# Performance work log

Hardware: AMD Instinct MI355X
Metric: run time of the kernel (lower is better)

Reference implementation:

```python
import jax, jax.numpy as jnp
import numpy as np

L = 10          # number of integration steps
MU = 0.02       # residual intensity weight
SIGMA = 2.0     # Gaussian RKHS sigma (voxels)
KS = 13         # kernel size ~ 2*ceil(3*sigma)+1
SLOPE = 0.01    # LeakyReLU default negative slope
HID = 50


def _gauss1d():
    r = jnp.arange(KS, dtype=jnp.float32) - (KS - 1) / 2.0
    k = jnp.exp(-0.5 * (r / SIGMA) ** 2)
    return k / k.sum()


def gaussian_smooth(x):
    # x: [B,C,D,H,W]; separable Gaussian RKHS smoothing, zero ('constant') border
    B, C, D, H, W = x.shape
    k = _gauss1d().astype(x.dtype)
    y = x.reshape(B * C, 1, D, H, W)
    p = (KS - 1) // 2
    dn = ('NCDHW', 'OIDHW', 'NCDHW')
    y = jax.lax.conv_general_dilated(y, k.reshape(1, 1, KS, 1, 1), (1, 1, 1), [(p, p), (0, 0), (0, 0)], dimension_numbers=dn)
    y = jax.lax.conv_general_dilated(y, k.reshape(1, 1, 1, KS, 1), (1, 1, 1), [(0, 0), (p, p), (0, 0)], dimension_numbers=dn)
    y = jax.lax.conv_general_dilated(y, k.reshape(1, 1, 1, 1, KS), (1, 1, 1), [(0, 0), (0, 0), (p, p)], dimension_numbers=dn)
    return y.reshape(B, C, D, H, W)


def spatial_gradient_3d(img):
    # img [B,1,D,H,W] -> [B,1,3,D,H,W]; central differences, replicate pad; channels (d/dx=W, d/dy=H, d/dz=D)
    def cd(axis):
        pad = [(0, 0)] * 5
        pad[axis] = (1, 1)
        p = jnp.pad(img, pad, mode='edge')
        sp = [slice(None)] * 5
        sm = [slice(None)] * 5
        sp[axis] = slice(2, None)
        sm[axis] = slice(0, -2)
        return 0.5 * (p[tuple(sp)] - p[tuple(sm)])
    return jnp.stack([cd(4), cd(3), cd(2)], axis=2)


def grid_sample_3d(img, grid):
    # trilinear grid_sample, align_corners=True, border padding
    # img [B,C,D,H,W]; grid [B,Do,Ho,Wo,3] with normalized (x,y,z) -> (W,H,D)
    B, C, D, H, W = img.shape
    Do, Ho, Wo = grid.shape[1:4]
    x = jnp.clip((grid[..., 0] + 1.0) * 0.5 * (W - 1), 0.0, W - 1.0)
    y = jnp.clip((grid[..., 1] + 1.0) * 0.5 * (H - 1), 0.0, H - 1.0)
    z = jnp.clip((grid[..., 2] + 1.0) * 0.5 * (D - 1), 0.0, D - 1.0)
    x0 = jnp.floor(x); y0 = jnp.floor(y); z0 = jnp.floor(z)
    x1 = jnp.minimum(x0 + 1.0, W - 1.0)
    y1 = jnp.minimum(y0 + 1.0, H - 1.0)
    z1 = jnp.minimum(z0 + 1.0, D - 1.0)
    wx = x - x0; wy = y - y0; wz = z - z0
    imgf = img.reshape(B, C, D * H * W)

    def gather(zi, yi, xi):
        idx = ((zi * H + yi) * W + xi).astype(jnp.int32).reshape(B, 1, -1)
        return jnp.take_along_axis(imgf, idx, axis=2)

    out = 0.0
    for zi, wzc in ((z0, 1.0 - wz), (z1, wz)):
        for yi, wyc in ((y0, 1.0 - wy), (y1, wy)):
            for xi, wxc in ((x0, 1.0 - wx), (x1, wx)):
                w8 = (wzc * wyc * wxc).reshape(B, 1, -1)
                out = out + gather(zi, yi, xi) * w8
    return out.reshape(B, C, Do, Ho, Wo)


def conv3d(x, w):
    return jax.lax.conv_general_dilated(x, w, (1, 1, 1), [(1, 1)] * 3, dimension_numbers=('NCDHW', 'OIDHW', 'NCDHW'))


def res_block(w1, w2, w3, z, I, J):
    # dropout is identity at inference
    x = jnp.concatenate([z, I, J], axis=1)
    x = jax.nn.leaky_relu(conv3d(x, w1), SLOPE)
    x = jax.nn.leaky_relu(conv3d(x, w2), SLOPE)
    return conv3d(x, w3)


def identity_grid(D, H, W):
    xs = jnp.linspace(-1.0, 1.0, W)
    ys = jnp.linspace(-1.0, 1.0, H)
    zs = jnp.linspace(-1.0, 1.0, D)
    zg, yg, xg = jnp.meshgrid(zs, ys, xs, indexing='ij')
    return jnp.stack([xg, yg, zg], axis=-1)[None]  # [1,D,H,W,3]


def metamorph_forward(source, target, source_seg, z0, W1, W2, W3):
    B = source.shape[0]
    D, H, W = source.shape[2:]
    id_grid = identity_grid(D, H, W)
    residual = jnp.broadcast_to(z0, (B,) + z0.shape[1:])
    res_def = jnp.zeros_like(source)
    phi = jnp.broadcast_to(id_grid, (B, D, H, W, 3))
    image = source
    fields, grads, residuals = [], [], [residual]
    for i in range(L):
        g = spatial_gradient_3d(image)                 # [B,1,3,D,H,W]
        grads.append(g)
        v = gaussian_smooth(-residual * g[:, 0])       # [B,3,D,H,W]
        field = jnp.transpose(v, (0, 4, 3, 2, 1))      # [B,W,H,D,3] (cubic volume)
        deformation = id_grid - field / L
        f = res_block(W1[i], W2[i], W3[i], residual, image, target) / L
        residual = residual + f
        residuals.append(residual)
        if i > 0:
            res_def = grid_sample_3d(res_def, deformation)
        res_def = res_def + residual
        phi = jnp.transpose(grid_sample_3d(jnp.transpose(phi, (0, 4, 3, 2, 1)), deformation), (0, 4, 3, 2, 1))
        mask = grid_sample_3d(source_seg, phi)
        image = grid_sample_3d(source, phi) + res_def * (MU ** 2 / L) * mask
        fields.append(field)
    return image, jnp.stack(fields), jnp.stack(grads), jnp.stack(residuals), res_def


def setup_inputs() -> dict:
    key = jax.random.key(0)
    ks = jax.random.split(key, 7)
    B, D = 1, 64
    return {
        "source": jax.random.normal(ks[0], (B, 1, D, D, D), jnp.float32),
        "target": jax.random.normal(ks[1], (B, 1, D, D, D), jnp.float32),
        "source_seg": jax.random.uniform(ks[2], (B, 1, D, D, D), jnp.float32),
        "z0": 0.1 * jax.random.normal(ks[3], (1, 1, D, D, D), jnp.float32),
        "W1": 0.05 * jax.random.normal(ks[4], (L, HID, 3, 3, 3, 3), jnp.float32),
        "W2": 0.05 * jax.random.normal(ks[5], (L, HID, HID, 3, 3, 3), jnp.float32),
        "W3": 0.05 * jax.random.normal(ks[6], (L, 1, HID, 3, 3, 3), jnp.float32),
    }


def reference(source, target, source_seg, z0, W1, W2, W3):
    return metamorph_forward(source, target, source_seg, z0, W1, W2, W3)
```

## Files before the change

### kernel.cpp

```cpp
#include <hip/hip_runtime.h>

#define NV 262144

using bf16x8 = __attribute__((ext_vector_type(8))) short;
using f32x4  = __attribute__((ext_vector_type(4))) float;

typedef const __attribute__((address_space(1))) unsigned int* gua_t;
typedef __attribute__((address_space(3))) unsigned int* lua_t;

static __device__ __forceinline__ void gld16(const void* g, void* l) {
  __builtin_amdgcn_global_load_lds((gua_t)g, (lua_t)l, 16, 0, 0);
}

static __device__ __forceinline__ unsigned short f2bf(float x) {
  unsigned int u = __float_as_uint(x);
  unsigned int r = (u + 0x7FFFu + ((u >> 16) & 1u)) >> 16;
  return (unsigned short)r;
}

static __device__ __forceinline__ void gauss_weights(float K[13]) {
  float s = 0.f;
#pragma unroll
  for (int j = 0; j < 13; ++j) {
    float r = (float)(j - 6);
    K[j] = expf(-0.125f * r * r);
    s += K[j];
  }
#pragma unroll
  for (int j = 0; j < 13; ++j) K[j] = K[j] / s;
}

static __device__ __forceinline__ void tl_make(float gx, float gy, float gz,
                                               int sx, int sy, int sz,
                                               int id[8], float wt[8]) {
  float x = fminf(fmaxf((gx + 1.0f) * 0.5f * 63.0f, 0.0f), 63.0f);
  float y = fminf(fmaxf((gy + 1.0f) * 0.5f * 63.0f, 0.0f), 63.0f);
  float z = fminf(fmaxf((gz + 1.0f) * 0.5f * 63.0f, 0.0f), 63.0f);
  float x0f = floorf(x), y0f = floorf(y), z0f = floorf(z);
  int x0 = (int)x0f, y0 = (int)y0f, z0 = (int)z0f;
  int x1 = min(x0 + 1, 63), y1 = min(y0 + 1, 63), z1 = min(z0 + 1, 63);
  float wx = x - x0f, wy = y - y0f, wz = z - z0f;
  float ux = 1.f - wx, uy = 1.f - wy, uz = 1.f - wz;
  int X0 = x0 * sx, X1 = x1 * sx, Y0 = y0 * sy, Y1 = y1 * sy, Z0 = z0 * sz, Z1 = z1 * sz;
  id[0] = Z0 + Y0 + X0; wt[0] = uz * uy * ux;
  id[1] = Z0 + Y0 + X1; wt[1] = uz * uy * wx;
  id[2] = Z0 + Y1 + X0; wt[2] = uz * wy * ux;
  id[3] = Z0 + Y1 + X1; wt[3] = uz * wy * wx;
  id[4] = Z1 + Y0 + X0; wt[4] = wz * uy * ux;
  id[5] = Z1 + Y0 + X1; wt[5] = wz * uy * wx;
  id[6] = Z1 + Y1 + X0; wt[6] = wz * wy * ux;
  id[7] = Z1 + Y1 + X1; wt[7] = wz * wy * wx;
}

static __device__ __forceinline__ float tl_apply(const float* __restrict__ img,
                                                 const int id[8], const float wt[8]) {
  float s = 0.f;
#pragma unroll
  for (int k = 0; k < 8; ++k) s = fmaf(wt[k], img[id[k]], s);
  return s;
}

__global__ void init_kernel(const float* __restrict__ src, const float* __restrict__ tgt,
                            const float* __restrict__ z0,
                            float* __restrict__ residual, float* __restrict__ image,
                            float* __restrict__ rd0, float* __restrict__ phi0,
                            float* __restrict__ outRes0, unsigned short* __restrict__ cinb,
                            float* __restrict__ zpf) {
  int idx = blockIdx.x * 256 + threadIdx.x;
  int d = idx >> 12, h = (idx >> 6) & 63, w = idx & 63;
  float z = z0[idx];
  float sv = src[idx];
  residual[idx] = z;
  outRes0[idx] = z;
  image[idx] = sv;
  rd0[idx] = 0.f;
  const float step = 2.0f / 63.0f;
  phi0[idx] = -1.f + w * step;
  phi0[NV + idx] = -1.f + h * step;
  phi0[2 * NV + idx] = -1.f + d * step;
  unsigned int u0 = (unsigned int)f2bf(z) | ((unsigned int)f2bf(sv) << 16);
  unsigned int u1 = (unsigned int)f2bf(tgt[idx]);
  *(uint2*)(cinb + (size_t)idx * 4) = make_uint2(u0, u1);
  if (idx < 32) zpf[idx] = 0.f;
}

__global__ void gsd_kernel(const float* __restrict__ img, const float* __restrict__ residual,
                           float* __restrict__ gout, float* __restrict__ t1) {
  int idx = blockIdx.x * 256 + threadIdx.x;
  int d = idx >> 12, h = (idx >> 6) & 63, w = idx & 63;
  float K[13]; gauss_weights(K);
  int wp = min(w + 1, 63), wm = max(w - 1, 0);
  int hp = min(h + 1, 63), hm = max(h - 1, 0);
  float a0 = 0.f, a1 = 0.f, a2 = 0.f;
#pragma unroll
  for (int j = 0; j < 13; ++j) {
    int dd = d + j - 6;
    if ((unsigned)dd < 64u) {
      int b = (dd << 12) + (h << 6);
      int dp = min(dd + 1, 63), dm = max(dd - 1, 0);
      float gx = 0.5f * (img[b + wp] - img[b + wm]);
      float gy = 0.5f * (img[(dd << 12) + (hp << 6) + w] - img[(dd << 12) + (hm << 6) + w]);
      float gz = 0.5f * (img[(dp << 12) + (h << 6) + w] - img[(dm << 12) + (h << 6) + w]);
      float r = residual[b + w];
      if (j == 6) {
        gout[idx] = gx; gout[NV + idx] = gy; gout[2 * NV + idx] = gz;
      }
      a0 = fmaf(K[j], -r * gx, a0);
      a1 = fmaf(K[j], -r * gy, a1);
      a2 = fmaf(K[j], -r * gz, a2);
    }
  }
  t1[idx] = a0; t1[NV + idx] = a1; t1[2 * NV + idx] = a2;
}

__global__ __launch_bounds__(256) void smooth_hw(const float* __restrict__ t1,
                                                 float* __restrict__ vbuf,
                                                 float* __restrict__ fout) {
  __shared__ float shin[16][64];
  __shared__ float shh[4][64];
  int w = threadIdx.x & 63;
  int ty = threadIdx.x >> 6;
  int h0 = blockIdx.x * 4;
  int d  = blockIdx.y;
  float K[13]; gauss_weights(K);
  for (int c = 0; c < 3; ++c) {
    __syncthreads();
    const float* tc = t1 + (size_t)c * NV + (d << 12);
    for (int r = ty; r < 16; r += 4) {
      int hh = h0 - 6 + r;
      shin[r][w] = ((unsigned)hh < 64u) ? tc[(hh << 6) + w] : 0.f;
    }
    __syncthreads();
    float acc = 0.f;
#pragma unroll
    for (int j = 0; j < 13; ++j) {
      int hh = h0 + ty + j - 6;
      if ((unsigned)hh < 64u) acc = fmaf(K[j], shin[ty + j][w], acc);
    }
    shh[ty][w] = acc;
    __syncthreads();
    float o = 0.f;
#pragma unroll
    for (int j = 0; j < 13; ++j) {
      int wj = w + j - 6;
      if ((unsigned)wj < 64u) o = fmaf(K[j], shh[ty][wj], o);
    }
    int h = h0 + ty;
    vbuf[(size_t)c * NV + (d << 12) + (h << 6) + w] = o;
    fout[((size_t)(w << 12) + (h << 6) + d) * 3 + c] = o;
  }
}

#define MFMA_PREP_G(XB, ZP)                                                        \
  const unsigned short* gp[6];                                                     \
  _Pragma("unroll")                                                                \
  for (int k = 0; k < 6; ++k) {                                                    \
    int S = wv * 384 + k * 64 + lane;                                              \
    int wws = S % 18; int t = S / 18; int q = t & 1; int dhh = t >> 1;             \
    int hh = dhh % 6; int dd = dhh / 6;                                            \
    int gz = d0 + dd - 1, gy = h0 + hh - 1, gx = w0 + wws - 1;                     \
    bool ok = (S < 1296) && ((unsigned)gz < 64u) && ((unsigned)gy < 64u) && ((unsigned)gx < 64u); \
    gp[k] = ok ? ((XB) + ((((gz << 12) + (gy << 6) + gx) << 6) + q * 8)) : (ZP);   \
  }

#define MFMA_ISSUE(G, DSTBUF)                                                      \
  _Pragma("unroll")                                                                \
  for (int k = 0; k < 6; ++k)                                                      \
    gld16(gp[k] + (G) * 16, (DSTBUF) + wv * 6144 + k * 1024);

#define TAP_ADDR                                                                   \
  int tap = 2 * c + (kb >> 1);                                                     \
  int tapc = min(tap, 26);                                                         \
  int kd = (tapc * 57) >> 9;                                                       \
  int rem = tapc - kd * 9;                                                         \
  int kh = (rem * 43) >> 7;                                                        \
  int kw = rem - kh * 3;                                                           \
  int rb = ((kd * 6 + kh) * 2 + (kb & 1)) * 288 + kw * 16;

#define MFMA_BLOCKID                                                               \
  int f = blockIdx.x + 4 * (blockIdx.y + 16 * blockIdx.z);                         \
  int nid = (f & 7) * 128 + (f >> 3);                                              \
  const int w0 = (nid & 3) * 16, h0 = ((nid >> 2) & 15) * 4, d0 = (nid >> 6) * 4;

#define MFMA_EPILOGUE(ACC, XOUT)                                                   \
  _Pragma("unroll")                                                                \
  for (int nf = 0; nf < 4; ++nf) {                                                 \
    int idx = ((d0 + wv) << 12) + ((h0 + nf) << 6) + (w0 + ww);                    \
    unsigned int base = (unsigned int)idx * 64u + kb * 4u;                         \
    _Pragma("unroll")                                                              \
    for (int mf = 0; mf < 4; ++mf) {                                               \
      float v0 = ACC[mf][nf][0], v1 = ACC[mf][nf][1];                              \
      float v2 = ACC[mf][nf][2], v3 = ACC[mf][nf][3];                              \
      v0 = (v0 >= 0.f) ? v0 : 0.01f * v0;                                          \
      v1 = (v1 >= 0.f) ? v1 : 0.01f * v1;                                          \
      v2 = (v2 >= 0.f) ? v2 : 0.01f * v2;                                          \
      v3 = (v3 >= 0.f) ? v3 : 0.01f * v3;                                          \
      unsigned int u0 = (unsigned int)f2bf(v0) | ((unsigned int)f2bf(v1) << 16);   \
      unsigned int u1 = (unsigned int)f2bf(v2) | ((unsigned int)f2bf(v3) << 16);   \
      *(uint2*)((XOUT) + base + mf * 16u) = make_uint2(u0, u1);                    \
    }                                                                              \
  }

__global__ __launch_bounds__(256) void conv1_mfma(const unsigned short* __restrict__ cinb,
                                                  const unsigned short* __restrict__ w1m,
                                                  unsigned short* __restrict__ x1b) {
  __shared__ char sh[1296 * 8];
  const int tid = threadIdx.x;
  const int lane = tid & 63;
  const int wv = tid >> 6;
  const int ww = lane & 15;
  const int kb = lane >> 4;
  MFMA_BLOCKID

  int gofs[6]; int lofs[6]; bool gok[6]; bool sval[6];
#pragma unroll
  for (int k = 0; k < 6; ++k) {
    int s = tid + k * 256;
    sval[k] = (s < 1296);
    int wws = s % 18; int rest = s / 18;
    int hh = rest % 6; int dd = rest / 6;
    int gz = d0 + dd - 1, gy = h0 + hh - 1, gx = w0 + wws - 1;
    bool ok = sval[k] && ((unsigned)gz < 64u) && ((unsigned)gy < 64u) && ((unsigned)gx < 64u);
    gok[k] = ok;
    gofs[k] = ok ? (((gz << 12) + (gy << 6) + gx) * 4) : 0;
    lofs[k] = s * 8;
  }
  {
    uint2 stg[6];
#pragma unroll
    for (int k = 0; k < 6; ++k)
      stg[k] = gok[k] ? *(const uint2*)(cinb + gofs[k]) : make_uint2(0u, 0u);
#pragma unroll
    for (int k = 0; k < 6; ++k)
      if (sval[k]) *(uint2*)(sh + lofs[k]) = stg[k];
  }
  __syncthreads();

  f32x4 acc[4][4];
#pragma unroll
  for (int mf = 0; mf < 4; ++mf)
#pragma unroll
    for (int nf = 0; nf < 4; ++nf) acc[mf][nf] = (f32x4)0.f;

#pragma unroll
  for (int g = 0; g < 4; ++g) {
    bf16x8 a0 = *(const bf16x8*)(w1m + (((g * 4 + 0) * 64 + lane) << 3));
    bf16x8 a1 = *(const bf16x8*)(w1m + (((g * 4 + 1) * 64 + lane) << 3));
    bf16x8 a2 = *(const bf16x8*)(w1m + (((g * 4 + 2) * 64 + lane) << 3));
    bf16x8 a3 = *(const bf16x8*)(w1m + (((g * 4 + 3) * 64 + lane) << 3));
    int tap0 = 8 * g + 2 * kb;
    int t0 = min(tap0, 26), t1 = min(tap0 + 1, 26);
    int kd0 = (t0 * 57) >> 9; int r0 = t0 - kd0 * 9; int kh0 = (r0 * 43) >> 7; int kw0 = r0 - kh0 * 3;
    int kd1 = (t1 * 57) >> 9; int r1 = t1 - kd1 * 9; int kh1 = (r1 * 43) >> 7; int kw1 = r1 - kh1 * 3;
#pragma unroll
    for (int nf = 0; nf < 4; ++nf) {
      union { uint2 u[2]; bf16x8 v; } bb;
      bb.u[0] = *(const uint2*)(sh + (((wv + kd0) * 6 + (nf + kh0)) * 18 + (ww + kw0)) * 8);
      bb.u[1] = *(const uint2*)(sh + (((wv + kd1) * 6 + (nf + kh1)) * 18 + (ww + kw1)) * 8);
      acc[0][nf] = __builtin_amdgcn_mfma_f32_16x16x32_bf16(a0, bb.v, acc[0][nf], 0, 0, 0);
      acc[1][nf] = __builtin_amdgcn_mfma_f32_16x16x32_bf16(a1, bb.v, acc[1][nf], 0, 0, 0);
      acc[2][nf] = __builtin_amdgcn_mfma_f32_16x16x32_bf16(a2, bb.v, acc[2][nf], 0, 0, 0);
      acc[3][nf] = __builtin_amdgcn_mfma_f32_16x16x32_bf16(a3, bb.v, acc[3][nf], 0, 0, 0);
    }
  }

  MFMA_EPILOGUE(acc, x1b)
}

__global__ __launch_bounds__(256) void conv2_mfma(const unsigned short* __restrict__ x1b,
                                                  const unsigned short* __restrict__ wtm,
                                                  unsigned short* __restrict__ x2b,
                                                  const unsigned short* __restrict__ zp) {
  __shared__ char sh[2][24576];
  const int tid = threadIdx.x;
  const int lane = tid & 63;
  const int wv = tid >> 6;
  const int ww = lane & 15;
  const int kb = lane >> 4;
  MFMA_BLOCKID

  MFMA_PREP_G(x1b, zp)

  f32x4 acc[4][4];
#pragma unroll
  for (int mf = 0; mf < 4; ++mf)
#pragma unroll
    for (int nf = 0; nf < 4; ++nf) acc[mf][nf] = (f32x4)0.f;

  const int nb0 = wv * 3456 + ww * 16;

  MFMA_ISSUE(0, sh[0])
  __syncthreads();

  for (int g = 0; g < 4; ++g) {
    if (g < 3) { MFMA_ISSUE(g + 1, sh[(g + 1) & 1]) }
    const char* buf = sh[g & 1];
#pragma unroll
    for (int c = 0; c < 14; ++c) {
      bf16x8 a0 = *(const bf16x8*)(wtm + ((((g * 14 + c) * 4 + 0) * 64 + lane) << 3));
      bf16x8 a1 = *(const bf16x8*)(wtm + ((((g * 14 + c) * 4 + 1) * 64 + lane) << 3));
      bf16x8 a2 = *(const bf16x8*)(wtm + ((((g * 14 + c) * 4 + 2) * 64 + lane) << 3));
      bf16x8 a3 = *(const bf16x8*)(wtm + ((((g * 14 + c) * 4 + 3) * 64 + lane) << 3));
      TAP_ADDR
      const char* bp = buf + nb0 + rb;
      bf16x8 b0 = *(const bf16x8*)(bp);
      bf16x8 b1 = *(const bf16x8*)(bp + 576);
      bf16x8 b2 = *(const bf16x8*)(bp + 2 * 576);
      bf16x8 b3 = *(const bf16x8*)(bp + 3 * 576);
#define MFMA_ROW(MF, AF)                                                              \
      acc[MF][0] = __builtin_amdgcn_mfma_f32_16x16x32_bf16(AF, b0, acc[MF][0], 0, 0, 0); \
      acc[MF][1] = __builtin_amdgcn_mfma_f32_16x16x32_bf16(AF, b1, acc[MF][1], 0, 0, 0); \
      acc[MF][2] = __builtin_amdgcn_mfma_f32_16x16x32_bf16(AF, b2, acc[MF][2], 0, 0, 0); \
      acc[MF][3] = __builtin_amdgcn_mfma_f32_16x16x32_bf16(AF, b3, acc[MF][3], 0, 0, 0);
      MFMA_ROW(0, a0)
      MFMA_ROW(1, a1)
      MFMA_ROW(2, a2)
      MFMA_ROW(3, a3)
#undef MFMA_ROW
    }
    __syncthreads();
  }

  MFMA_EPILOGUE(acc, x2b)
}

__global__ __launch_bounds__(256) void conv3_mfma(const unsigned short* __restrict__ x2b,
                                                  const unsigned short* __restrict__ w3m,
                                                  float* __restrict__ residual,
                                                  float* __restrict__ resOut,
                                                  const unsigned short* __restrict__ zp) {
  __shared__ char sh[2][24576];
  const int tid = threadIdx.x;
  const int lane = tid & 63;
  const int wv = tid >> 6;
  const int ww = lane & 15;
  const int kb = lane >> 4;
  MFMA_BLOCKID

  MFMA_PREP_G(x2b, zp)

  f32x4 acc[4];
#pragma unroll
  for (int nf = 0; nf < 4; ++nf) acc[nf] = (f32x4)0.f;

  const int nb0 = wv * 3456 + ww * 16;

  MFMA_ISSUE(0, sh[0])
  __syncthreads();

  for (int g = 0; g < 4; ++g) {
    if (g < 3) { MFMA_ISSUE(g + 1, sh[(g + 1) & 1]) }
    const char* buf = sh[g & 1];
#pragma unroll
    for (int c = 0; c < 14; ++c) {
      bf16x8 a0 = *(const bf16x8*)(w3m + (((g * 14 + c) * 64 + lane) << 3));
      TAP_ADDR
      const char* bp = buf + nb0 + rb;
      bf16x8 b0 = *(const bf16x8*)(bp);
      bf16x8 b1 = *(const bf16x8*)(bp + 576);
      bf16x8 b2 = *(const bf16x8*)(bp + 2 * 576);
      bf16x8 b3 = *(const bf16x8*)(bp + 3 * 576);
      acc[0] = __builtin_amdgcn_mfma_f32_16x16x32_bf16(a0, b0, acc[0], 0, 0, 0);
      acc[1] = __builtin_amdgcn_mfma_f32_16x16x32_bf16(a0, b1, acc[1], 0, 0, 0);
      acc[2] = __builtin_amdgcn_mfma_f32_16x16x32_bf16(a0, b2, acc[2], 0, 0, 0);
      acc[3] = __builtin_amdgcn_mfma_f32_16x16x32_bf16(a0, b3, acc[3], 0, 0, 0);
    }
    __syncthreads();
  }

  if (lane < 16) {
#pragma unroll
    for (int nf = 0; nf < 4; ++nf) {
      int idx = ((d0 + wv) << 12) + ((h0 + nf) << 6) + (w0 + ww);
      float nr = residual[idx] + acc[nf][0] * 0.1f;
      residual[idx] = nr;
      resOut[idx] = nr;
    }
  }
}

__global__ void rp_fused_kernel(const float* __restrict__ rdOld, const float* __restrict__ v,
                                const float* __restrict__ residual,
                                const float* __restrict__ phiOld, float* __restrict__ phiNew,
                                const float* __restrict__ src, const float* __restrict__ seg,
                                const float* __restrict__ tgt,
                                float* __restrict__ rdNew, float* __restrict__ image,
                                unsigned short* __restrict__ cinb, int doSample) {
  int idx = blockIdx.x * 256 + threadIdx.x;
  int d = idx >> 12, h = (idx >> 6) & 63, w = idx & 63;
  const float step = 2.0f / 63.0f;
  float rres = residual[idx];

  float val = 0.f;
  if (doSample) {
    int tidx = (w << 12) + (h << 6) + d;
    float gx = (-1.f + w * step) - v[tidx] / 10.0f;
    float gy = (-1.f + h * step) - v[NV + tidx] / 10.0f;
    float gz = (-1.f + d * step) - v[2 * NV + tidx] / 10.0f;
    int id[8]; float wt[8];
    tl_make(gx, gy, gz, 1, 64, 4096, id, wt);
    val = tl_apply(rdOld, id, wt);
  }
  float nr = val + rres;
  rdNew[idx] = nr;

  float gx = (-1.f + d * step) - v[idx] / 10.0f;
  float gy = (-1.f + h * step) - v[NV + idx] / 10.0f;
  float gz = (-1.f + w * step) - v[2 * NV + idx] / 10.0f;
  int id[8]; float wt[8];
  tl_make(gx, gy, gz, 4096, 64, 1, id, wt);
  float px = tl_apply(phiOld, id, wt);
  float py = tl_apply(phiOld + NV, id, wt);
  float pz = tl_apply(phiOld + 2 * NV, id, wt);
  phiNew[idx] = px;
  phiNew[NV + idx] = py;
  phiNew[2 * NV + idx] = pz;

  int id2[8]; float wt2[8];
  tl_make(px, py, pz, 1, 64, 4096, id2, wt2);
  float sval = tl_apply(src, id2, wt2);
  float mval = tl_apply(seg, id2, wt2);
  float img = sval + nr * 4.0e-05f * mval;
  image[idx] = img;

  unsigned int u0 = (unsigned int)f2bf(rres) | ((unsigned int)f2bf(img) << 16);
  unsigned int u1 = (unsigned int)f2bf(tgt[idx]);
  *(uint2*)(cinb + (size_t)idx * 4) = make_uint2(u0, u1);
}

__global__ void w1m_kernel(const float* __restrict__ W1, unsigned short* __restrict__ w1m) {
  int gid = blockIdx.x * 256 + threadIdx.x;
  if (gid >= 10 * 4 * 4 * 64 * 8) return;
  int j = gid & 7;
  int l = (gid >> 3) & 63;
  int mf = (gid >> 9) & 3;
  int g = (gid >> 11) & 3;
  int i = gid >> 13;
  int m = mf * 16 + (l & 15);
  int kb = l >> 4;
  int k = 32 * g + 8 * kb + j;
  int tap = k >> 2;
  int ci = k & 3;
  float v = 0.f;
  if (m < 50 && tap < 27 && ci < 3)
    v = W1[(((size_t)i * 50 + m) * 3 + ci) * 27 + tap];
  w1m[gid] = f2bf(v);
}

__global__ void wt2m_kernel(const float* __restrict__ W2, unsigned short* __restrict__ wtm) {
  int gid = blockIdx.x * 256 + threadIdx.x;
  if (gid >= 10 * 4 * 14 * 4 * 64 * 8) return;
  int j = gid & 7;
  int l = (gid >> 3) & 63;
  int mf = (gid >> 9) & 3;
  int rest = gid >> 11;
  int c = rest % 14; rest /= 14;
  int g = rest & 3;  int i = rest >> 2;
  int m = mf * 16 + (l & 15);
  int kb = l >> 4;
  int klocal = c * 32 + kb * 8 + j;
  int tap = klocal >> 4;
  int cil = klocal & 15;
  int ci = g * 16 + cil;
  float v = 0.f;
  if (tap < 27 && ci < 50 && m < 50)
    v = W2[(((size_t)i * 50 + m) * 50 + ci) * 27 + tap];
  wtm[gid] = f2bf(v);
}

__global__ void w3m_kernel(const float* __restrict__ W3, unsigned short* __restrict__ w3m) {
  int gid = blockIdx.x * 256 + threadIdx.x;
  if (gid >= 10 * 4 * 14 * 64 * 8) return;
  int j = gid & 7;
  int l = (gid >> 3) & 63;
  int rest = gid >> 9;
  int c = rest % 14; rest /= 14;
  int g = rest & 3;  int i = rest >> 2;
  int m = l & 15;
  int kb = l >> 4;
  int klocal = c * 32 + kb * 8 + j;
  int tap = klocal >> 4;
  int cil = klocal & 15;
  int ci = g * 16 + cil;
  float v = 0.f;
  if (m == 0 && tap < 27 && ci < 50)
    v = W3[((size_t)i * 50 + ci) * 27 + tap];
  w3m[gid] = f2bf(v);
}

extern "C" void kernel_launch(void* const* d_in, const int* in_sizes, int n_in,
                              void* d_out, int out_size, void* d_ws, size_t ws_size,
                              hipStream_t stream) {
  const float* src = (const float*)d_in[0];
  const float* tgt = (const float*)d_in[1];
  const float* seg = (const float*)d_in[2];
  const float* z0  = (const float*)d_in[3];
  const float* W1  = (const float*)d_in[4];
  const float* W2  = (const float*)d_in[5];
  const float* W3  = (const float*)d_in[6];
  float* out = (float*)d_out;
  float* ws = (float*)d_ws;

  const size_t N = NV;
  float* residual = ws;
  float* image    = ws + N;
  float* rdb[2]   = { ws + 2 * N, ws + 3 * N };
  float* phib[2]  = { ws + 4 * N, ws + 7 * N };
  float* vbuf     = ws + 10 * N;
  float* t1       = ws + 13 * N;
  unsigned short* cinb = (unsigned short*)(ws + 16 * N);
  unsigned short* x1b = (unsigned short*)(ws + 19 * N);
  unsigned short* x2b = (unsigned short*)(ws + 51 * N);
  unsigned short* wt2m = (unsigned short*)(ws + 83 * N);
  unsigned short* w3m  = wt2m + (size_t)10 * 4 * 14 * 4 * 64 * 8;
  unsigned short* w1m  = w3m + (size_t)10 * 4 * 14 * 64 * 8;
  unsigned short* zp   = w1m + (size_t)10 * 4 * 4 * 64 * 8;

  size_t needed = 83 * N * sizeof(float)
                + ((size_t)10 * 4 * 14 * 4 * 64 * 8 + (size_t)10 * 4 * 14 * 64 * 8
                   + (size_t)10 * 4 * 4 * 64 * 8) * 2 + 128;
  if (ws_size < needed) return;

  float* out_image  = out;
  float* out_fields = out + N;
  float* out_grads  = out + 31 * N;
  float* out_resid  = out + 61 * N;
  float* out_rd     = out + 72 * N;

  dim3 blk(256);
  dim3 grdN((unsigned)(N / 256));
  dim3 sgrd(16, 64);
  dim3 m1grd(4, 16, 16);

  init_kernel<<<grdN, blk, 0, stream>>>(src, tgt, z0, residual, image, rdb[0], phib[0],
                                        out_resid, cinb, (float*)zp);
  w1m_kernel<<<(10 * 4 * 4 * 64 * 8 + 255) / 256, blk, 0, stream>>>(W1, w1m);
  wt2m_kernel<<<(10 * 4 * 14 * 4 * 64 * 8 + 255) / 256, blk, 0, stream>>>(W2, wt2m);
  w3m_kernel<<<(10 * 4 * 14 * 64 * 8 + 255) / 256, blk, 0, stream>>>(W3, w3m);

  int rc = 0, pc = 0;
  for (int i = 0; i < 10; ++i) {
    gsd_kernel<<<grdN, blk, 0, stream>>>(image, residual, out_grads + (size_t)i * 3 * N, t1);
    smooth_hw<<<sgrd, blk, 0, stream>>>(t1, vbuf, out_fields + (size_t)i * 3 * N);

    conv1_mfma<<<m1grd, blk, 0, stream>>>(cinb, w1m + (size_t)i * 4 * 4 * 64 * 8, x1b);
    conv2_mfma<<<m1grd, blk, 0, stream>>>(x1b, wt2m + (size_t)i * 4 * 14 * 4 * 64 * 8, x2b, zp);
    conv3_mfma<<<m1grd, blk, 0, stream>>>(x2b, w3m + (size_t)i * 4 * 14 * 64 * 8, residual,
                                          out_resid + (size_t)(i + 1) * N, zp);

    float* rdNew = (i == 9) ? out_rd : rdb[1 - rc];
    float* imgNew = (i == 9) ? out_image : image;
    rp_fused_kernel<<<grdN, blk, 0, stream>>>(rdb[rc], vbuf, residual, phib[pc],
                                              phib[1 - pc], src, seg, tgt, rdNew, imgNew,
                                              cinb, i > 0 ? 1 : 0);
    rc = 1 - rc;
    pc = 1 - pc;
  }
}
```

Before: 1.518 ms.

## Regroup conv2/conv3 reduction into 8-channel groups with 4 taps per chunk

Restructures the K dimension of the conv2 and conv3 MFMA kernels from 4 groups of 16 channels (2 taps per 32-wide chunk) to 7 groups of 8 channels (4 taps per chunk), with matching weight repacking. This reduces padded channel work from 64 to 56 channels, cutting MFMA count and global-to-LDS staging, and halves LDS buffer size. In exchange it adds more pipeline stages and barriers per block.

```diff
diff --git a/kernel.cpp b/kernel.cpp
--- a/kernel.cpp
+++ b/kernel.cpp
@@ -151,31 +151,31 @@
   }
 }
 
-#define MFMA_PREP_G(XB, ZP)                                                        \
-  const unsigned short* gp[6];                                                     \
+#define MFMA_PREP_G7(XB, ZP)                                                       \
+  const unsigned short* gp[3];                                                     \
   _Pragma("unroll")                                                                \
-  for (int k = 0; k < 6; ++k) {                                                    \
-    int S = wv * 384 + k * 64 + lane;                                              \
-    int wws = S % 18; int t = S / 18; int q = t & 1; int dhh = t >> 1;             \
-    int hh = dhh % 6; int dd = dhh / 6;                                            \
+  for (int k = 0; k < 3; ++k) {                                                    \
+    int S = wv * 192 + k * 64 + lane;                                              \
+    int wws = S % 18; int t = S / 18;                                              \
+    int hh = t % 6; int dd = t / 6;                                                \
     int gz = d0 + dd - 1, gy = h0 + hh - 1, gx = w0 + wws - 1;                     \
-    bool ok = (S < 1296) && ((unsigned)gz < 64u) && ((unsigned)gy < 64u) && ((unsigned)gx < 64u); \
-    gp[k] = ok ? ((XB) + ((((gz << 12) + (gy << 6) + gx) << 6) + q * 8)) : (ZP);   \
-  }
-
-#define MFMA_ISSUE(G, DSTBUF)                                                      \
+    bool ok = (S < 648) && ((unsigned)gz < 64u) && ((unsigned)gy < 64u) && ((unsigned)gx < 64u); \
+    gp[k] = ok ? ((XB) + (((gz << 12) + (gy << 6) + gx) << 6)) : (ZP);             \
+  }
+
+#define MFMA_ISSUE7(G, DSTBUF)                                                     \
   _Pragma("unroll")                                                                \
-  for (int k = 0; k < 6; ++k)                                                      \
-    gld16(gp[k] + (G) * 16, (DSTBUF) + wv * 6144 + k * 1024);
-
-#define TAP_ADDR                                                                   \
-  int tap = 2 * c + (kb >> 1);                                                     \
+  for (int k = 0; k < 3; ++k)                                                      \
+    gld16(gp[k] + (G) * 8, (DSTBUF) + wv * 3072 + k * 1024);
+
+#define TAP_ADDR7                                                                  \
+  int tap = 4 * c + kb;                                                            \
   int tapc = min(tap, 26);                                                         \
   int kd = (tapc * 57) >> 9;                                                       \
   int rem = tapc - kd * 9;                                                         \
   int kh = (rem * 43) >> 7;                                                        \
   int kw = rem - kh * 3;                                                           \
-  int rb = ((kd * 6 + kh) * 2 + (kb & 1)) * 288 + kw * 16;
+  int rb = kd * 1728 + kh * 288 + kw * 16;
 
 #define MFMA_BLOCKID                                                               \
   int f = blockIdx.x + 4 * (blockIdx.y + 16 * blockIdx.z);                         \
@@ -271,7 +271,7 @@
                                                   const unsigned short* __restrict__ wtm,
                                                   unsigned short* __restrict__ x2b,
                                                   const unsigned short* __restrict__ zp) {
-  __shared__ char sh[2][24576];
+  __shared__ char sh[2][12288];
   const int tid = threadIdx.x;
   const int lane = tid & 63;
   const int wv = tid >> 6;
@@ -279,7 +279,7 @@
   const int kb = lane >> 4;
   MFMA_BLOCKID
 
-  MFMA_PREP_G(x1b, zp)
+  MFMA_PREP_G7(x1b, zp)
 
   f32x4 acc[4][4];
 #pragma unroll
@@ -287,26 +287,26 @@
 #pragma unroll
     for (int nf = 0; nf < 4; ++nf) acc[mf][nf] = (f32x4)0.f;
 
-  const int nb0 = wv * 3456 + ww * 16;
-
-  MFMA_ISSUE(0, sh[0])
+  const int nb0 = wv * 1728 + ww * 16;
+
+  MFMA_ISSUE7(0, sh[0])
   __syncthreads();
 
-  for (int g = 0; g < 4; ++g) {
-    if (g < 3) { MFMA_ISSUE(g + 1, sh[(g + 1) & 1]) }
+  for (int g = 0; g < 7; ++g) {
+    if (g < 6) { MFMA_ISSUE7(g + 1, sh[(g + 1) & 1]) }
     const char* buf = sh[g & 1];
 #pragma unroll
-    for (int c = 0; c < 14; ++c) {
-      bf16x8 a0 = *(const bf16x8*)(wtm + ((((g * 14 + c) * 4 + 0) * 64 + lane) << 3));
-      bf16x8 a1 = *(const bf16x8*)(wtm + ((((g * 14 + c) * 4 + 1) * 64 + lane) << 3));
-      bf16x8 a2 = *(const bf16x8*)(wtm + ((((g * 14 + c) * 4 + 2) * 64 + lane) << 3));
-      bf16x8 a3 = *(const bf16x8*)(wtm + ((((g * 14 + c) * 4 + 3) * 64 + lane) << 3));
-      TAP_ADDR
+    for (int c = 0; c < 7; ++c) {
+      bf16x8 a0 = *(const bf16x8*)(wtm + ((((g * 7 + c) * 4 + 0) * 64 + lane) << 3));
+      bf16x8 a1 = *(const bf16x8*)(wtm + ((((g * 7 + c) * 4 + 1) * 64 + lane) << 3));
+      bf16x8 a2 = *(const bf16x8*)(wtm + ((((g * 7 + c) * 4 + 2) * 64 + lane) << 3));
+      bf16x8 a3 = *(const bf16x8*)(wtm + ((((g * 7 + c) * 4 + 3) * 64 + lane) << 3));
+      TAP_ADDR7
       const char* bp = buf + nb0 + rb;
       bf16x8 b0 = *(const bf16x8*)(bp);
-      bf16x8 b1 = *(const bf16x8*)(bp + 576);
-      bf16x8 b2 = *(const bf16x8*)(bp + 2 * 576);
-      bf16x8 b3 = *(const bf16x8*)(bp + 3 * 576);
+      bf16x8 b1 = *(const bf16x8*)(bp + 288);
+      bf16x8 b2 = *(const bf16x8*)(bp + 2 * 288);
+      bf16x8 b3 = *(const bf16x8*)(bp + 3 * 288);
 #define MFMA_ROW(MF, AF)                                                              \
       acc[MF][0] = __builtin_amdgcn_mfma_f32_16x16x32_bf16(AF, b0, acc[MF][0], 0, 0, 0); \
       acc[MF][1] = __builtin_amdgcn_mfma_f32_16x16x32_bf16(AF, b1, acc[MF][1], 0, 0, 0); \
@@ -329,7 +329,7 @@
                                                   float* __restrict__ residual,
                                                   float* __restrict__ resOut,
                                                   const unsigned short* __restrict__ zp) {
-  __shared__ char sh[2][24576];
+  __shared__ char sh[2][12288];
   const int tid = threadIdx.x;
   const int lane = tid & 63;
   const int wv = tid >> 6;
@@ -337,29 +337,29 @@
   const int kb = lane >> 4;
   MFMA_BLOCKID
 
-  MFMA_PREP_G(x2b, zp)
+  MFMA_PREP_G7(x2b, zp)
 
   f32x4 acc[4];
 #pragma unroll
   for (int nf = 0; nf < 4; ++nf) acc[nf] = (f32x4)0.f;
 
-  const int nb0 = wv * 3456 + ww * 16;
-
-  MFMA_ISSUE(0, sh[0])
+  const int nb0 = wv * 1728 + ww * 16;
+
+  MFMA_ISSUE7(0, sh[0])
   __syncthreads();
 
-  for (int g = 0; g < 4; ++g) {
-    if (g < 3) { MFMA_ISSUE(g + 1, sh[(g + 1) & 1]) }
+  for (int g = 0; g < 7; ++g) {
+    if (g < 6) { MFMA_ISSUE7(g + 1, sh[(g + 1) & 1]) }
     const char* buf = sh[g & 1];
 #pragma unroll
-    for (int c = 0; c < 14; ++c) {
-      bf16x8 a0 = *(const bf16x8*)(w3m + (((g * 14 + c) * 64 + lane) << 3));
-      TAP_ADDR
+    for (int c = 0; c < 7; ++c) {
+      bf16x8 a0 = *(const bf16x8*)(w3m + (((g * 7 + c) * 64 + lane) << 3));
+      TAP_ADDR7
       const char* bp = buf + nb0 + rb;
       bf16x8 b0 = *(const bf16x8*)(bp);
-      bf16x8 b1 = *(const bf16x8*)(bp + 576);
-      bf16x8 b2 = *(const bf16x8*)(bp + 2 * 576);
-      bf16x8 b3 = *(const bf16x8*)(bp + 3 * 576);
+      bf16x8 b1 = *(const bf16x8*)(bp + 288);
+      bf16x8 b2 = *(const bf16x8*)(bp + 2 * 288);
+      bf16x8 b3 = *(const bf16x8*)(bp + 3 * 288);
       acc[0] = __builtin_amdgcn_mfma_f32_16x16x32_bf16(a0, b0, acc[0], 0, 0, 0);
       acc[1] = __builtin_amdgcn_mfma_f32_16x16x32_bf16(a0, b1, acc[1], 0, 0, 0);
       acc[2] = __builtin_amdgcn_mfma_f32_16x16x32_bf16(a0, b2, acc[2], 0, 0, 0);
@@ -449,19 +449,17 @@
 
 __global__ void wt2m_kernel(const float* __restrict__ W2, unsigned short* __restrict__ wtm) {
   int gid = blockIdx.x * 256 + threadIdx.x;
-  if (gid >= 10 * 4 * 14 * 4 * 64 * 8) return;
+  if (gid >= 10 * 7 * 7 * 4 * 64 * 8) return;
   int j = gid & 7;
   int l = (gid >> 3) & 63;
   int mf = (gid >> 9) & 3;
   int rest = gid >> 11;
-  int c = rest % 14; rest /= 14;
-  int g = rest & 3;  int i = rest >> 2;
+  int c = rest % 7; rest /= 7;
+  int g = rest % 7; int i = rest / 7;
   int m = mf * 16 + (l & 15);
   int kb = l >> 4;
-  int klocal = c * 32 + kb * 8 + j;
-  int tap = klocal >> 4;
-  int cil = klocal & 15;
-  int ci = g * 16 + cil;
+  int tap = 4 * c + kb;
+  int ci = 8 * g + j;
   float v = 0.f;
   if (tap < 27 && ci < 50 && m < 50)
     v = W2[(((size_t)i * 50 + m) * 50 + ci) * 27 + tap];
@@ -470,18 +468,16 @@
 
 __global__ void w3m_kernel(const float* __restrict__ W3, unsigned short* __restrict__ w3m) {
   int gid = blockIdx.x * 256 + threadIdx.x;
-  if (gid >= 10 * 4 * 14 * 64 * 8) return;
+  if (gid >= 10 * 7 * 7 * 64 * 8) return;
   int j = gid & 7;
   int l = (gid >> 3) & 63;
   int rest = gid >> 9;
-  int c = rest % 14; rest /= 14;
-  int g = rest & 3;  int i = rest >> 2;
+  int c = rest % 7; rest /= 7;
+  int g = rest % 7; int i = rest / 7;
   int m = l & 15;
   int kb = l >> 4;
-  int klocal = c * 32 + kb * 8 + j;
-  int tap = klocal >> 4;
-  int cil = klocal & 15;
-  int ci = g * 16 + cil;
+  int tap = 4 * c + kb;
+  int ci = 8 * g + j;
   float v = 0.f;
   if (m == 0 && tap < 27 && ci < 50)
     v = W3[((size_t)i * 50 + ci) * 27 + tap];
@@ -502,6 +498,10 @@
   float* ws = (float*)d_ws;
 
   const size_t N = NV;
+  const size_t WT2M = (size_t)10 * 7 * 7 * 4 * 64 * 8;
+  const size_t W3M  = (size_t)10 * 7 * 7 * 64 * 8;
+  const size_t W1M  = (size_t)10 * 4 * 4 * 64 * 8;
+
   float* residual = ws;
   float* image    = ws + N;
   float* rdb[2]   = { ws + 2 * N, ws + 3 * N };
@@ -512,13 +512,11 @@
   unsigned short* x1b = (unsigned short*)(ws + 19 * N);
   unsigned short* x2b = (unsigned short*)(ws + 51 * N);
   unsigned short* wt2m = (unsigned short*)(ws + 83 * N);
-  unsigned short* w3m  = wt2m + (size_t)10 * 4 * 14 * 4 * 64 * 8;
-  unsigned short* w1m  = w3m + (size_t)10 * 4 * 14 * 64 * 8;
-  unsigned short* zp   = w1m + (size_t)10 * 4 * 4 * 64 * 8;
-
-  size_t needed = 83 * N * sizeof(float)
-                + ((size_t)10 * 4 * 14 * 4 * 64 * 8 + (size_t)10 * 4 * 14 * 64 * 8
-                   + (size_t)10 * 4 * 4 * 64 * 8) * 2 + 128;
+  unsigned short* w3m  = wt2m + WT2M;
+  unsigned short* w1m  = w3m + W3M;
+  unsigned short* zp   = w1m + W1M;
+
+  size_t needed = 83 * N * sizeof(float) + (WT2M + W3M + W1M) * 2 + 128;
   if (ws_size < needed) return;
 
   float* out_image  = out;
@@ -534,9 +532,9 @@
 
   init_kernel<<<grdN, blk, 0, stream>>>(src, tgt, z0, residual, image, rdb[0], phib[0],
                                         out_resid, cinb, (float*)zp);
-  w1m_kernel<<<(10 * 4 * 4 * 64 * 8 + 255) / 256, blk, 0, stream>>>(W1, w1m);
-  wt2m_kernel<<<(10 * 4 * 14 * 4 * 64 * 8 + 255) / 256, blk, 0, stream>>>(W2, wt2m);
-  w3m_kernel<<<(10 * 4 * 14 * 64 * 8 + 255) / 256, blk, 0, stream>>>(W3, w3m);
+  w1m_kernel<<<(int)((W1M + 255) / 256), blk, 0, stream>>>(W1, w1m);
+  wt2m_kernel<<<(int)((WT2M + 255) / 256), blk, 0, stream>>>(W2, wt2m);
+  w3m_kernel<<<(int)((W3M + 255) / 256), blk, 0, stream>>>(W3, w3m);
 
   int rc = 0, pc = 0;
   for (int i = 0; i < 10; ++i) {
@@ -544,8 +542,8 @@
     smooth_hw<<<sgrd, blk, 0, stream>>>(t1, vbuf, out_fields + (size_t)i * 3 * N);
 
     conv1_mfma<<<m1grd, blk, 0, stream>>>(cinb, w1m + (size_t)i * 4 * 4 * 64 * 8, x1b);
-    conv2_mfma<<<m1grd, blk, 0, stream>>>(x1b, wt2m + (size_t)i * 4 * 14 * 4 * 64 * 8, x2b, zp);
-    conv3_mfma<<<m1grd, blk, 0, stream>>>(x2b, w3m + (size_t)i * 4 * 14 * 64 * 8, residual,
+    conv2_mfma<<<m1grd, blk, 0, stream>>>(x1b, wt2m + (size_t)i * 7 * 7 * 4 * 64 * 8, x2b, zp);
+    conv3_mfma<<<m1grd, blk, 0, stream>>>(x2b, w3m + (size_t)i * 7 * 7 * 64 * 8, residual,
                                           out_resid + (size_t)(i + 1) * N, zp);
 
     float* rdNew = (i == 9) ? out_rd : rdb[1 - rc];
```

Result: faster. 1.403 ms (-7.6%).
